# Performance work log

Measured on AMD Instinct MI355X. Metric: run time of the kernel, lower is better.

The kernel has to match this reference:

```python
import jax, jax.numpy as jnp
import numpy as np

B, C, H, W = 64, 256, 28, 28
EPS = 1e-8  # torch CosineSimilarity eps


def _make_grids(key):
    # coordinate meshgrid [2, H, W]: channel 0 = y, channel 1 = x
    yy, xx = jnp.meshgrid(jnp.arange(H, dtype=jnp.float32),
                          jnp.arange(W, dtype=jnp.float32), indexing='ij')
    coords = jnp.stack([yy, xx])  # [2, H, W]
    k1, k2 = jax.random.split(key)
    scale = jax.random.uniform(k1, (B, 1, 1, 1), minval=0.9, maxval=1.1)
    shift = jax.random.uniform(k2, (B, 2, 1, 1), minval=0.0, maxval=5.0)
    return coords[None] * scale + shift  # [B, 2, H, W]


def setup_inputs() -> dict:
    key = jax.random.key(0)
    ks = jax.random.split(key, 6)
    return {
        'y1': jax.random.normal(ks[0], (B, C, H, W), jnp.float32),
        'y2': jax.random.normal(ks[1], (B, C, H, W), jnp.float32),
        'z1': jax.random.normal(ks[2], (B, C, H, W), jnp.float32),
        'z2': jax.random.normal(ks[3], (B, C, H, W), jnp.float32),
        'view1_grid': _make_grids(ks[4]),
        'view2_grid': _make_grids(ks[5]),
    }


def _grid_distances(grid1, grid2):
    # grid*: [B, 2, H, W] -> [B, 2, N]; pairwise euclidean dist [B, N, N]
    g1 = grid1.reshape(grid1.shape[0], 2, -1)
    g2 = grid2.reshape(grid2.shape[0], 2, -1)
    dy = g1[:, 0, :, None] - g2[:, 0, None, :]
    dx = g1[:, 1, :, None] - g2[:, 1, None, :]
    return jnp.sqrt(dy * dy + dx * dx)


def _cosine_sim_pairwise(a, b):
    # a, b: [B, C, N]; cosine sim over channel dim -> [B, N, N]
    num = jnp.einsum('bcn,bcm->bnm', a, b)
    na = jnp.linalg.norm(a, axis=1)  # [B, N]
    nb = jnp.linalg.norm(b, axis=1)  # [B, N]
    den = jnp.maximum(na[:, :, None] * nb[:, None, :], EPS)
    return num / den


def _masked_mean(sim, mask):
    m = mask.astype(sim.dtype)
    return jnp.sum(sim * m) / jnp.sum(m)


def reference(y1, y2, z1, z2, view1_grid, view2_grid):
    distance_thr = 0.7
    y1f = y1.reshape(y1.shape[0], y1.shape[1], -1)
    y2f = y2.reshape(y2.shape[0], y2.shape[1], -1)
    z1f = z1.reshape(z1.shape[0], z1.shape[1], -1)
    z2f = z2.reshape(z2.shape[0], z2.shape[1], -1)

    distances = _grid_distances(view1_grid, view2_grid)  # [B, N, N]
    view1_bin = jnp.linalg.norm(view1_grid[..., 1, 1] - view1_grid[..., 0, 0], axis=-1)  # [B]
    view2_bin = jnp.linalg.norm(view2_grid[..., 1, 1] - view2_grid[..., 0, 0], axis=-1)  # [B]

    view1_mask = (distances / view1_bin[:, None, None]) <= distance_thr
    view2_mask = (distances / view2_bin[:, None, None]) <= distance_thr

    view1_loss = _masked_mean(_cosine_sim_pairwise(y1f, z2f), view1_mask)
    view2_loss = _masked_mean(_cosine_sim_pairwise(y2f, z1f), view2_mask)
    return -1.0 * (view1_loss + view2_loss)
```

## Files before the change

kernel.cpp:

```cpp
#include <hip/hip_runtime.h>
#include <hip/hip_bf16.h>

#define BB   64
#define CC   256
#define NPIX 784
#define BNP  (BB * NPIX)
#define SLOTS 128

__global__ __launch_bounds__(512, 8) void zt_k(
    const float* __restrict__ z1, const float* __restrict__ z2,
    float* __restrict__ zt, float* __restrict__ zn2) {
    __shared__ float lds[32 * 257];
    __shared__ float part[16][32];

    int bx = blockIdx.x;
    int nt = bx % 25;
    int t  = bx / 25;
    int b  = t & 63;
    int arr = t >> 6;
    int nlim = (nt == 24) ? 16 : 32;

    const float* in = (arr ? z2 : z1) + (size_t)b * CC * NPIX + nt * 32;
    int tid  = threadIdx.x;
    int n4   = tid & 7;
    int subc = tid >> 3;
    int nn   = 4 * n4;

#pragma unroll
    for (int k = 0; k < 4; k++) {
        int c = subc + 64 * k;
        float4 v = {0.f, 0.f, 0.f, 0.f};
        if (nn < nlim) v = *(const float4*)(in + (size_t)c * NPIX + nn);
        lds[(nn + 0) * 257 + c] = v.x;
        lds[(nn + 1) * 257 + c] = v.y;
        lds[(nn + 2) * 257 + c] = v.z;
        lds[(nn + 3) * 257 + c] = v.w;
    }
    __syncthreads();

    {
        int nl = tid & 31, cq = tid >> 5;
        float s = 0.f;
#pragma unroll
        for (int sc = 0; sc < 16; sc++) {
            float v = lds[nl * 257 + cq * 16 + sc];
            s = fmaf(v, v, s);
        }
        part[cq][nl] = s;
    }

    float* outb = zt + ((size_t)arr * BB + b) * ((size_t)NPIX * CC)
                     + (size_t)nt * 32 * CC;
    int lane = tid & 63, wv = tid >> 6;
    int c4 = lane & 15, nq = (lane >> 4) & 3;
    int n = 4 * wv + nq;
    if (n < nlim) {
#pragma unroll
        for (int cq2 = 0; cq2 < 4; cq2++) {
            int cc0 = 64 * cq2 + 4 * c4;
            float4 v;
            v.x = lds[n * 257 + cc0 + 0];
            v.y = lds[n * 257 + cc0 + 1];
            v.z = lds[n * 257 + cc0 + 2];
            v.w = lds[n * 257 + cc0 + 3];
            *(float4*)(outb + (size_t)n * CC + cc0) = v;
        }
    }
    __syncthreads();
    if (tid < nlim) {
        float s = 0.f;
#pragma unroll
        for (int k = 0; k < 16; k++) s += part[k][tid];
        zn2[(size_t)arr * BNP + (size_t)b * NPIX + nt * 32 + tid] = s;
    }
}

__global__ __launch_bounds__(1024, 8) void pairs_k(
    const float* __restrict__ y1, const float* __restrict__ y2,
    const float* __restrict__ zt, const float* __restrict__ zn2,
    const float* __restrict__ g1g, const float* __restrict__ g2g,
    double* __restrict__ acc) {
    __shared__ float  ylds[16 * 256];
    __shared__ double shs[16];
    __shared__ int    shc[16];

    int tid  = threadIdx.x;
    int lane = tid & 63, wv = tid >> 6;
    int bx   = blockIdx.x;
    int loss = (bx >= 3136) ? 1 : 0;
    int rem  = bx - loss * 3136;
    int b    = rem / 49;
    int ig   = rem - b * 49;
    int i0   = 16 * ig;

    const float* Yg = (loss ? y2 : y1) + (size_t)b * CC * NPIX;
    if (tid < 256) {
        const float* row = Yg + (size_t)tid * NPIX + i0;
#pragma unroll
        for (int q = 0; q < 4; q++) {
            float4 v = *(const float4*)(row + 4 * q);
            ylds[(4 * q + 0) * 256 + tid] = v.x;
            ylds[(4 * q + 1) * 256 + tid] = v.y;
            ylds[(4 * q + 2) * 256 + tid] = v.z;
            ylds[(4 * q + 3) * 256 + tid] = v.w;
        }
    }

    const float* g1 = g1g + (size_t)b * 2 * NPIX;
    const float* g2 = g2g + (size_t)b * 2 * NPIX;
    int i = i0 + wv;
    float g1y = g1[i];
    float g1x = g1[NPIX + i];

    const float* gb = loss ? g2 : g1;
    float d0  = gb[29] - gb[0];
    float d1  = gb[NPIX + 29] - gb[NPIX];
    float bin = __fsqrt_rn(__fadd_rn(__fmul_rn(d0, d0), __fmul_rn(d1, d1)));

    float t2y = g2[0], t2x = g2[NPIX];
    float s2y = g2[28] - g2[0];
    float s2x = g2[NPIX + 1] - g2[NPIX];
    float r  = 0.7f * bin * 1.0002f + 1e-4f;
    float cy = (g1y - t2y) / s2y;
    float cx = (g1x - t2x) / s2x;
    float ry = r / s2y + 0.05f;
    float rx = r / s2x + 0.05f;
    int jy0 = max(0,  (int)ceilf(cy - ry));
    int jy1 = min(27, (int)floorf(cy + ry));
    int jx0 = max(0,  (int)ceilf(cx - rx));
    int jx1 = min(27, (int)floorf(cx + rx));
    int dyr = jy1 - jy0, dxr = jx1 - jx0;

    int dyl = lane >> 2, dxl = lane & 3;
    bool pass = false;
    if (lane < 16 && dyl <= dyr && dxl <= dxr) {
        int jc = (jy0 + dyl) * 28 + jx0 + dxl;
        float dy = g1y - g2[jc];
        float dx = g1x - g2[NPIX + jc];
        float d  = __fsqrt_rn(__fadd_rn(__fmul_rn(dy, dy), __fmul_rn(dx, dx)));
        pass = (__fdiv_rn(d, bin) <= 0.7f);
    }
    unsigned long long m = __ballot(pass);
    int cnt = __builtin_popcountll(m);

    __syncthreads();

    int gl = lane & 15, g = lane >> 4;
    const float4* Yr = (const float4*)(ylds + wv * 256);
    float4 ya = Yr[gl], yb = Yr[gl + 16], yc = Yr[gl + 32], yd = Yr[gl + 48];

    float p = ya.x * ya.x;
    p = fmaf(ya.y, ya.y, p); p = fmaf(ya.z, ya.z, p); p = fmaf(ya.w, ya.w, p);
    p = fmaf(yb.x, yb.x, p); p = fmaf(yb.y, yb.y, p); p = fmaf(yb.z, yb.z, p);
    p = fmaf(yb.w, yb.w, p);
    p = fmaf(yc.x, yc.x, p); p = fmaf(yc.y, yc.y, p); p = fmaf(yc.z, yc.z, p);
    p = fmaf(yc.w, yc.w, p);
    p = fmaf(yd.x, yd.x, p); p = fmaf(yd.y, yd.y, p); p = fmaf(yd.z, yd.z, p);
    p = fmaf(yd.w, yd.w, p);
#pragma unroll
    for (int off = 1; off < 16; off <<= 1) p += __shfl_xor(p, off);
    float na = __fsqrt_rn(p);

    const float* Zb = zt  + ((size_t)(1 - loss) * BB + b) * ((size_t)NPIX * CC);
    const float* zn = zn2 + ((size_t)(1 - loss) * BB + b) * NPIX;

    unsigned mm = (unsigned)m;
    if (g > 0) mm &= mm - 1;
    if (g > 1) mm &= mm - 1;
    if (g > 2) mm &= mm - 1;
    int rounds = (cnt + 3) >> 2;

    double ssum = 0.0;
    for (int r = 0; r < rounds; r++) {
        bool val = (mm != 0);
        int s = val ? (__ffs(mm) - 1) : 0;
        int j = val ? ((jy0 + (s >> 2)) * 28 + jx0 + (s & 3)) : 0;
        const float4* Z4 = (const float4*)(Zb + (size_t)j * CC);
        float4 za = Z4[gl], zb_ = Z4[gl + 16], zc = Z4[gl + 32], zd = Z4[gl + 48];
        float nb2 = zn[j];
        float dp = ya.x * za.x;
        dp = fmaf(ya.y, za.y, dp); dp = fmaf(ya.z, za.z, dp);
        dp = fmaf(ya.w, za.w, dp);
        dp = fmaf(yb.x, zb_.x, dp); dp = fmaf(yb.y, zb_.y, dp);
        dp = fmaf(yb.z, zb_.z, dp); dp = fmaf(yb.w, zb_.w, dp);
        dp = fmaf(yc.x, zc.x, dp); dp = fmaf(yc.y, zc.y, dp);
        dp = fmaf(yc.z, zc.z, dp); dp = fmaf(yc.w, zc.w, dp);
        dp = fmaf(yd.x, zd.x, dp); dp = fmaf(yd.y, zd.y, dp);
        dp = fmaf(yd.z, zd.z, dp); dp = fmaf(yd.w, zd.w, dp);
#pragma unroll
        for (int off = 1; off < 16; off <<= 1) dp += __shfl_xor(dp, off);
        float den = fmaxf(na * __fsqrt_rn(nb2), 1e-8f);
        float sim = __fdividef(dp, den);
        if (val) ssum += (double)sim;
        mm &= mm - 1; mm &= mm - 1; mm &= mm - 1; mm &= mm - 1;
    }
    ssum += __shfl_xor(ssum, 16);
    ssum += __shfl_xor(ssum, 32);

    if (lane == 0) { shs[wv] = ssum; shc[wv] = cnt; }
    __syncthreads();
    if (tid == 0) {
        double s = 0.0; int c = 0;
#pragma unroll
        for (int k = 0; k < 16; k++) { s += shs[k]; c += shc[k]; }
        double* slot = acc + (size_t)(bx & (SLOTS - 1)) * 4;
        atomicAdd(&slot[loss * 2],     s);
        atomicAdd(&slot[loss * 2 + 1], (double)c);
    }
}

__global__ void fin_k(const double* __restrict__ acc, float* __restrict__ out) {
    int lane = threadIdx.x;
    double s0 = 0, m0 = 0, s1 = 0, m1 = 0;
    for (int s = lane; s < SLOTS; s += 64) {
        const double* p = acc + (size_t)s * 4;
        s0 += p[0]; m0 += p[1]; s1 += p[2]; m1 += p[3];
    }
#pragma unroll
    for (int off = 32; off; off >>= 1) {
        s0 += __shfl_xor(s0, off); m0 += __shfl_xor(m0, off);
        s1 += __shfl_xor(s1, off); m1 += __shfl_xor(m1, off);
    }
    if (lane == 0) out[0] = (float)(-(s0 / m0 + s1 / m1));
}

extern "C" void kernel_launch(void* const* d_in, const int* in_sizes, int n_in,
                              void* d_out, int out_size, void* d_ws, size_t ws_size,
                              hipStream_t stream) {
    const float* y1 = (const float*)d_in[0];
    const float* y2 = (const float*)d_in[1];
    const float* z1 = (const float*)d_in[2];
    const float* z2 = (const float*)d_in[3];
    const float* g1 = (const float*)d_in[4];
    const float* g2 = (const float*)d_in[5];
    float* out = (float*)d_out;

    char* ws = (char*)d_ws;
    double* acc = (double*)ws;
    float*  zn2 = (float*)(ws + 4096);
    float*  zt  = (float*)(ws + 4096 + 2 * BNP * sizeof(float));

    hipMemsetAsync(acc, 0, SLOTS * 4 * sizeof(double), stream);

    zt_k<<<3200, 512, 0, stream>>>(z1, z2, zt, zn2);

    pairs_k<<<6272, 1024, 0, stream>>>(y1, y2, zt, zn2, g1, g2, acc);

    fin_k<<<1, 64, 0, stream>>>(acc, out);
}
```

Baseline: 267.5 us.

## Fuse z transpose into pairs kernel via per-tile LDS neighbor slab

Removes the separate transpose/norm kernel and its workspace round trip. Each block now handles a half-row of 14 query pixels and gathers the small 3x20 window of z neighbor pixels it can need straight from the original layout into shared memory, computing their norms in-block. Block indices are remapped so batches are grouped per XCD for cache locality. The cost is redundant strided scalar z gathers across blocks and a larger LDS footprint, which can lower occupancy.

```diff
diff --git a/kernel.cpp b/kernel.cpp
--- a/kernel.cpp
+++ b/kernel.cpp
@@ -1,134 +1,89 @@
 #include <hip/hip_runtime.h>
-#include <hip/hip_bf16.h>
 
 #define BB   64
 #define CC   256
 #define NPIX 784
-#define BNP  (BB * NPIX)
 #define SLOTS 128
 
-__global__ __launch_bounds__(512, 8) void zt_k(
+__global__ __launch_bounds__(896, 7) void pairs_k(
+    const float* __restrict__ y1, const float* __restrict__ y2,
     const float* __restrict__ z1, const float* __restrict__ z2,
-    float* __restrict__ zt, float* __restrict__ zn2) {
-    __shared__ float lds[32 * 257];
-    __shared__ float part[16][32];
-
-    int bx = blockIdx.x;
-    int nt = bx % 25;
-    int t  = bx / 25;
-    int b  = t & 63;
-    int arr = t >> 6;
-    int nlim = (nt == 24) ? 16 : 32;
-
-    const float* in = (arr ? z2 : z1) + (size_t)b * CC * NPIX + nt * 32;
-    int tid  = threadIdx.x;
-    int n4   = tid & 7;
-    int subc = tid >> 3;
-    int nn   = 4 * n4;
-
-#pragma unroll
-    for (int k = 0; k < 4; k++) {
-        int c = subc + 64 * k;
-        float4 v = {0.f, 0.f, 0.f, 0.f};
-        if (nn < nlim) v = *(const float4*)(in + (size_t)c * NPIX + nn);
-        lds[(nn + 0) * 257 + c] = v.x;
-        lds[(nn + 1) * 257 + c] = v.y;
-        lds[(nn + 2) * 257 + c] = v.z;
-        lds[(nn + 3) * 257 + c] = v.w;
-    }
-    __syncthreads();
-
-    {
-        int nl = tid & 31, cq = tid >> 5;
-        float s = 0.f;
-#pragma unroll
-        for (int sc = 0; sc < 16; sc++) {
-            float v = lds[nl * 257 + cq * 16 + sc];
-            s = fmaf(v, v, s);
-        }
-        part[cq][nl] = s;
-    }
-
-    float* outb = zt + ((size_t)arr * BB + b) * ((size_t)NPIX * CC)
-                     + (size_t)nt * 32 * CC;
-    int lane = tid & 63, wv = tid >> 6;
-    int c4 = lane & 15, nq = (lane >> 4) & 3;
-    int n = 4 * wv + nq;
-    if (n < nlim) {
-#pragma unroll
-        for (int cq2 = 0; cq2 < 4; cq2++) {
-            int cc0 = 64 * cq2 + 4 * c4;
-            float4 v;
-            v.x = lds[n * 257 + cc0 + 0];
-            v.y = lds[n * 257 + cc0 + 1];
-            v.z = lds[n * 257 + cc0 + 2];
-            v.w = lds[n * 257 + cc0 + 3];
-            *(float4*)(outb + (size_t)n * CC + cc0) = v;
-        }
-    }
-    __syncthreads();
-    if (tid < nlim) {
-        float s = 0.f;
-#pragma unroll
-        for (int k = 0; k < 16; k++) s += part[k][tid];
-        zn2[(size_t)arr * BNP + (size_t)b * NPIX + nt * 32 + tid] = s;
-    }
-}
-
-__global__ __launch_bounds__(1024, 8) void pairs_k(
-    const float* __restrict__ y1, const float* __restrict__ y2,
-    const float* __restrict__ zt, const float* __restrict__ zn2,
     const float* __restrict__ g1g, const float* __restrict__ g2g,
     double* __restrict__ acc) {
-    __shared__ float  ylds[16 * 256];
-    __shared__ double shs[16];
-    __shared__ int    shc[16];
+    __shared__ float  slab[60 * 260];
+    __shared__ float  ylds[14 * 256];
+    __shared__ float  nlds[60];
+    __shared__ double shs[14];
+    __shared__ int    shc[14];
 
     int tid  = threadIdx.x;
     int lane = tid & 63, wv = tid >> 6;
-    int bx   = blockIdx.x;
-    int loss = (bx >= 3136) ? 1 : 0;
-    int rem  = bx - loss * 3136;
-    int b    = rem / 49;
-    int ig   = rem - b * 49;
-    int i0   = 16 * ig;
-
-    const float* Yg = (loss ? y2 : y1) + (size_t)b * CC * NPIX;
-    if (tid < 256) {
-        const float* row = Yg + (size_t)tid * NPIX + i0;
-#pragma unroll
-        for (int q = 0; q < 4; q++) {
-            float4 v = *(const float4*)(row + 4 * q);
-            ylds[(4 * q + 0) * 256 + tid] = v.x;
-            ylds[(4 * q + 1) * 256 + tid] = v.y;
-            ylds[(4 * q + 2) * 256 + tid] = v.z;
-            ylds[(4 * q + 3) * 256 + tid] = v.w;
-        }
-    }
+    int bid  = blockIdx.x;
+    int xcd  = bid & 7;
+    int q    = bid >> 3;
+    int loss = q / 448;
+    int rr   = q - loss * 448;
+    int b8   = rr / 56;
+    int tile = rr - b8 * 56;
+    int b    = xcd + 8 * b8;
+    int row  = tile >> 1, hf = tile & 1;
+    int i0   = row * 28 + 14 * hf;
 
     const float* g1 = g1g + (size_t)b * 2 * NPIX;
     const float* g2 = g2g + (size_t)b * 2 * NPIX;
-    int i = i0 + wv;
-    float g1y = g1[i];
-    float g1x = g1[NPIX + i];
 
     const float* gb = loss ? g2 : g1;
     float d0  = gb[29] - gb[0];
     float d1  = gb[NPIX + 29] - gb[NPIX];
     float bin = __fsqrt_rn(__fadd_rn(__fmul_rn(d0, d0), __fmul_rn(d1, d1)));
-
     float t2y = g2[0], t2x = g2[NPIX];
     float s2y = g2[28] - g2[0];
     float s2x = g2[NPIX + 1] - g2[NPIX];
-    float r  = 0.7f * bin * 1.0002f + 1e-4f;
+    float rV  = 0.7f * bin * 1.0002f + 1e-4f;
+    float ryr = rV / s2y + 0.05f;
+    float rxr = rV / s2x + 0.05f;
+    float cy0 = (g1[i0] - t2y) / s2y;
+    int JR0 = max(0, (int)ceilf(cy0 - ryr));
+    float cxf = (g1[NPIX + i0] - t2x) / s2x;
+    int JCL = max(0, (int)ceilf(cxf - rxr));
+
+    const float* Zb = (loss ? z1 : z2) + (size_t)b * CC * NPIX;
+#pragma unroll
+    for (int m = 0; m < 18; m++) {
+        int idx = tid + 896 * m;
+        if (idx < 15360) {
+            int c  = idx / 60;
+            int s  = idx - c * 60;
+            int ry = (s >= 40) ? 2 : ((s >= 20) ? 1 : 0);
+            int k  = s - ry * 20;
+            int jr = min(JR0 + ry, 27);
+            int jc = min(JCL + k, 27);
+            slab[s * 260 + c] = Zb[(size_t)c * NPIX + jr * 28 + jc];
+        }
+    }
+
+    const float* Yg = (loss ? y2 : y1) + (size_t)b * CC * NPIX;
+#pragma unroll
+    for (int m = 0; m < 2; m++) {
+        int idx = tid + 896 * m;
+        if (idx < 1792) {
+            int c  = idx / 7;
+            int qq = idx - c * 7;
+            float2 v = *(const float2*)(Yg + (size_t)c * NPIX + i0 + 2 * qq);
+            ylds[(2 * qq + 0) * 256 + c] = v.x;
+            ylds[(2 * qq + 1) * 256 + c] = v.y;
+        }
+    }
+
+    int i = i0 + wv;
+    float g1y = g1[i];
+    float g1x = g1[NPIX + i];
     float cy = (g1y - t2y) / s2y;
     float cx = (g1x - t2x) / s2x;
-    float ry = r / s2y + 0.05f;
-    float rx = r / s2x + 0.05f;
-    int jy0 = max(0,  (int)ceilf(cy - ry));
-    int jy1 = min(27, (int)floorf(cy + ry));
-    int jx0 = max(0,  (int)ceilf(cx - rx));
-    int jx1 = min(27, (int)floorf(cx + rx));
+    int jy0 = max(0,  (int)ceilf(cy - ryr));
+    int jy1 = min(27, (int)floorf(cy + ryr));
+    int jx0 = max(0,  (int)ceilf(cx - rxr));
+    int jx1 = min(27, (int)floorf(cx + rxr));
     int dyr = jy1 - jy0, dxr = jx1 - jx0;
 
     int dyl = lane >> 2, dxl = lane & 3;
@@ -140,9 +95,30 @@
         float d  = __fsqrt_rn(__fadd_rn(__fmul_rn(dy, dy), __fmul_rn(dx, dx)));
         pass = (__fdiv_rn(d, bin) <= 0.7f);
     }
-    unsigned long long m = __ballot(pass);
-    int cnt = __builtin_popcountll(m);
-
+    unsigned long long mball = __ballot(pass);
+    int cnt = __builtin_popcountll(mball);
+
+    __syncthreads();
+
+    {
+        int gid = wv * 4 + (lane >> 4);
+        int gl2 = lane & 15;
+        for (int s = gid; s < 60; s += 56) {
+            const float4* Z4 = (const float4*)(slab + s * 260);
+            float4 a = Z4[gl2], b4 = Z4[gl2 + 16], c4 = Z4[gl2 + 32], e4 = Z4[gl2 + 48];
+            float pp = a.x * a.x;
+            pp = fmaf(a.y, a.y, pp); pp = fmaf(a.z, a.z, pp); pp = fmaf(a.w, a.w, pp);
+            pp = fmaf(b4.x, b4.x, pp); pp = fmaf(b4.y, b4.y, pp); pp = fmaf(b4.z, b4.z, pp);
+            pp = fmaf(b4.w, b4.w, pp);
+            pp = fmaf(c4.x, c4.x, pp); pp = fmaf(c4.y, c4.y, pp); pp = fmaf(c4.z, c4.z, pp);
+            pp = fmaf(c4.w, c4.w, pp);
+            pp = fmaf(e4.x, e4.x, pp); pp = fmaf(e4.y, e4.y, pp); pp = fmaf(e4.z, e4.z, pp);
+            pp = fmaf(e4.w, e4.w, pp);
+#pragma unroll
+            for (int off = 1; off < 16; off <<= 1) pp += __shfl_xor(pp, off);
+            if (gl2 == 0) nlds[s] = pp;
+        }
+    }
     __syncthreads();
 
     int gl = lane & 15, g = lane >> 4;
@@ -161,23 +137,21 @@
     for (int off = 1; off < 16; off <<= 1) p += __shfl_xor(p, off);
     float na = __fsqrt_rn(p);
 
-    const float* Zb = zt  + ((size_t)(1 - loss) * BB + b) * ((size_t)NPIX * CC);
-    const float* zn = zn2 + ((size_t)(1 - loss) * BB + b) * NPIX;
-
-    unsigned mm = (unsigned)m;
+    int off_i = jx0 - JCL;
+    unsigned mm = (unsigned)mball;
     if (g > 0) mm &= mm - 1;
     if (g > 1) mm &= mm - 1;
     if (g > 2) mm &= mm - 1;
     int rounds = (cnt + 3) >> 2;
 
     double ssum = 0.0;
-    for (int r = 0; r < rounds; r++) {
+    for (int r2 = 0; r2 < rounds; r2++) {
         bool val = (mm != 0);
-        int s = val ? (__ffs(mm) - 1) : 0;
-        int j = val ? ((jy0 + (s >> 2)) * 28 + jx0 + (s & 3)) : 0;
-        const float4* Z4 = (const float4*)(Zb + (size_t)j * CC);
+        int s  = val ? (__ffs(mm) - 1) : 0;
+        int sl = val ? ((s >> 2) * 20 + off_i + (s & 3)) : 0;
+        const float4* Z4 = (const float4*)(slab + sl * 260);
         float4 za = Z4[gl], zb_ = Z4[gl + 16], zc = Z4[gl + 32], zd = Z4[gl + 48];
-        float nb2 = zn[j];
+        float nb2 = nlds[sl];
         float dp = ya.x * za.x;
         dp = fmaf(ya.y, za.y, dp); dp = fmaf(ya.z, za.z, dp);
         dp = fmaf(ya.w, za.w, dp);
@@ -202,8 +176,8 @@
     if (tid == 0) {
         double s = 0.0; int c = 0;
 #pragma unroll
-        for (int k = 0; k < 16; k++) { s += shs[k]; c += shc[k]; }
-        double* slot = acc + (size_t)(bx & (SLOTS - 1)) * 4;
+        for (int k = 0; k < 14; k++) { s += shs[k]; c += shc[k]; }
+        double* slot = acc + (size_t)(bid & (SLOTS - 1)) * 4;
         atomicAdd(&slot[loss * 2],     s);
         atomicAdd(&slot[loss * 2 + 1], (double)c);
     }
@@ -235,16 +209,10 @@
     const float* g2 = (const float*)d_in[5];
     float* out = (float*)d_out;
 
-    char* ws = (char*)d_ws;
-    double* acc = (double*)ws;
-    float*  zn2 = (float*)(ws + 4096);
-    float*  zt  = (float*)(ws + 4096 + 2 * BNP * sizeof(float));
-
+    double* acc = (double*)d_ws;
     hipMemsetAsync(acc, 0, SLOTS * 4 * sizeof(double), stream);
 
-    zt_k<<<3200, 512, 0, stream>>>(z1, z2, zt, zn2);
-
-    pairs_k<<<6272, 1024, 0, stream>>>(y1, y2, zt, zn2, g1, g2, acc);
+    pairs_k<<<7168, 896, 0, stream>>>(y1, y2, z1, z2, g1, g2, acc);
 
     fin_k<<<1, 64, 0, stream>>>(acc, out);
 }
```

Result: slower. 517.0 us (+93.2%).
